# Kernel tuning notes

Measured on AMD Instinct MI355X. Metric: run time of the kernel, lower is better.

The kernel has to match this reference:

```python
import jax, jax.numpy as jnp
import numpy as np

D_MODEL = 2048
D_LATENT = 512
NUM_HEADS = 16
B, T = 2, 2048


def setup_inputs() -> dict:
    key = jax.random.key(0)
    ks = jax.random.split(key, 6)
    s = 0.02  # init scale
    return {
        "x": jax.random.normal(ks[0], (B, T, D_MODEL), jnp.float32),
        # weights stored as [in, out] so y = x @ W (== torch x @ weight.T)
        "w_dkv": jax.random.normal(ks[1], (D_MODEL, D_LATENT), jnp.float32) * s,
        # w_uk kept in torch weight layout [d_model, d_latent] for absorption
        "w_uk": jax.random.normal(ks[2], (D_MODEL, D_LATENT), jnp.float32) * s,
        "w_uv": jax.random.normal(ks[3], (D_LATENT, D_MODEL), jnp.float32) * s,
        "w_q": jax.random.normal(ks[4], (D_MODEL, D_MODEL), jnp.float32) * s,
        "w_o": jax.random.normal(ks[5], (D_MODEL, D_MODEL), jnp.float32) * s,
    }


def reference(x, w_dkv, w_uk, w_uv, w_q, w_o):
    # Eval-mode MLA with weight absorption (w_q_w_uk), dropout is a no-op.
    Bsz, Tl, C = x.shape
    H = NUM_HEADS
    S = C // H
    L = w_dkv.shape[1]
    scale = 1.0 / jnp.sqrt(jnp.asarray(C, x.dtype))

    kv_latent = x @ w_dkv  # [B,T,L]

    # absorbed projection: w_q.T.view(C,H,S) einsum w_uk.view(H,S,L) -> [H,C,L]
    absorbed = jnp.einsum('chs,hsl->hcl', w_q.reshape(C, H, S), w_uk.reshape(H, S, L))

    q_lat = jnp.einsum('btc,hcl->bhtl', x, absorbed)            # [B,H,T,L]
    att = jnp.einsum('bhtl,bsl->bhts', q_lat, kv_latent) * scale  # [B,H,T,T]

    causal_mask = jnp.triu(jnp.ones((Tl, Tl), bool), k=1)
    att = jnp.where(causal_mask, jnp.asarray(-jnp.inf, att.dtype), att)
    att = jax.nn.softmax(att, axis=-1)

    v = (kv_latent @ w_uv).reshape(Bsz, Tl, H, S)               # [B,T,H,S]
    y = jnp.einsum('bhts,bshd->bthd', att, v).reshape(Bsz, Tl, C)
    return y @ w_o
```

## Files before the change

### kernel.cpp

```cpp
#include <hip/hip_runtime.h>
#include <hip/hip_bf16.h>

#define T_SEQ 2048
#define C_DIM 2048
#define L_DIM 512
#define H_NUM 16
#define S_DIM 128
#define B_SZ  2

typedef __attribute__((ext_vector_type(8))) short bf16x8;
typedef __attribute__((ext_vector_type(4))) float f32x4;
typedef __attribute__((ext_vector_type(4))) short short4v;

__device__ inline short f2bf(float f) {
    union { float f; unsigned u; } x; x.f = f;
    unsigned r = x.u + 0x7fffu + ((x.u >> 16) & 1u);
    return (short)(r >> 16);
}

__device__ __forceinline__ void wtile_body(const float* __restrict__ in, short* __restrict__ out,
                                           int R, int C, int r0, int c0, int tid) {
    __shared__ float lds[64][66];
    #pragma unroll
    for (int it = 0; it < 4; it++) {
        int r = (tid >> 4) + it * 16;
        int c4 = (tid & 15) * 4;
        float4 v = *(const float4*)&in[(long)(r0 + r) * C + c0 + c4];
        lds[c4 + 0][r] = v.x; lds[c4 + 1][r] = v.y;
        lds[c4 + 2][r] = v.z; lds[c4 + 3][r] = v.w;
    }
    __syncthreads();
    #pragma unroll
    for (int it = 0; it < 4; it++) {
        int c = tid >> 2;
        int rb = (tid & 3) * 16 + it * 4;
        short4v o;
        #pragma unroll
        for (int j = 0; j < 4; j++) o[j] = f2bf(lds[c][rb + j]);
        *(short4v*)&out[(long)(c0 + c) * R + r0 + rb] = o;
    }
}

__global__ __launch_bounds__(256) void prep_kernel(
    const float* __restrict__ x, short* __restrict__ xb,
    const float* __restrict__ wq, short* __restrict__ wqT,
    const float* __restrict__ wdkv, short* __restrict__ wdkvT,
    const float* __restrict__ wuk, short* __restrict__ wukT,
    const float* __restrict__ wuv, short* __restrict__ wuvT,
    const float* __restrict__ wo, short* __restrict__ woT)
{
    int bid = blockIdx.x, tid = threadIdx.x;
    if (bid < 8192) {
        int i = bid * 256 + tid;
        float4 v = ((const float4*)x)[i];
        short4v o;
        o[0] = f2bf(v.x); o[1] = f2bf(v.y); o[2] = f2bf(v.z); o[3] = f2bf(v.w);
        ((short4v*)xb)[i] = o;
        return;
    }
    int t = bid - 8192;
    if (t < 1024)       wtile_body(wq,   wqT,   2048, 2048, (t >> 5) * 64,            (t & 31) * 64, tid);
    else if (t < 1280)  wtile_body(wdkv, wdkvT, 2048, 512,  ((t - 1024) >> 3) * 64,   ((t - 1024) & 7) * 64, tid);
    else if (t < 1536)  wtile_body(wuk,  wukT,  2048, 512,  ((t - 1280) >> 3) * 64,   ((t - 1280) & 7) * 64, tid);
    else if (t < 1792)  wtile_body(wuv,  wuvT,  512,  2048, ((t - 1536) >> 5) * 64,   ((t - 1536) & 31) * 64, tid);
    else                wtile_body(wo,   woT,   2048, 2048, ((t - 1792) >> 5) * 64,   ((t - 1792) & 31) * 64, tid);
}

__global__ __launch_bounds__(256) void vtrans_kernel(const short* __restrict__ v,
                                                     short* __restrict__ vt) {
    __shared__ short lds[64][68];
    int id = blockIdx.x;
    int b = id >> 10, t2 = id & 1023;
    int t0 = (t2 >> 5) * 64, c0 = (t2 & 31) * 64;
    const short* in = v + (long)b * T_SEQ * C_DIM;
    short* out = vt + (long)b * T_SEQ * C_DIM;
    int tid = threadIdx.x;
    #pragma unroll
    for (int it = 0; it < 4; it++) {
        int t = (tid >> 4) + it * 16;
        int c4 = (tid & 15) * 4;
        short4v vv = *(const short4v*)&in[(long)(t0 + t) * C_DIM + c0 + c4];
        lds[c4 + 0][t] = vv[0]; lds[c4 + 1][t] = vv[1];
        lds[c4 + 2][t] = vv[2]; lds[c4 + 3][t] = vv[3];
    }
    __syncthreads();
    #pragma unroll
    for (int it = 0; it < 4; it++) {
        int c = tid >> 2;
        int tb = (tid & 3) * 16 + it * 4;
        short4v o = *(const short4v*)&lds[c][tb];
        *(short4v*)&out[(long)(c0 + c) * C_DIM + t0 + tb] = o;
    }
}

__device__ __forceinline__ void gemm_body(
    const short* __restrict__ A, const short* __restrict__ Bt,
    float* __restrict__ Cf, short* __restrict__ Cb,
    int K, int lda, int ldb, int ldc, int m0, int n0, long coff, bool outf32, float cscale,
    short (&As)[2][128 * 32], short (&Bs)[2][128 * 32])
{
    int tid = threadIdx.x;
    int wave = tid >> 6, l = tid & 63;
    int wm = (wave >> 1) * 64, wn = (wave & 1) * 64;
    int lr = l & 15, lhi = l >> 4;
    f32x4 acc[4][4] = {};

#define STAGE_AB(KI, BUF) do { \
        _Pragma("unroll") \
        for (int r = 0; r < 2; r++) { \
            int e = (r * 256 + tid) * 8; \
            int row = e >> 5, col = e & 31; \
            __builtin_amdgcn_global_load_lds( \
                (const __attribute__((address_space(1))) unsigned int*)(A + (long)(m0 + row) * lda + (KI) * 32 + col), \
                (__attribute__((address_space(3))) unsigned int*)(&As[BUF][e]), 16, 0, 0); \
            __builtin_amdgcn_global_load_lds( \
                (const __attribute__((address_space(1))) unsigned int*)(Bt + (long)(n0 + row) * ldb + (KI) * 32 + col), \
                (__attribute__((address_space(3))) unsigned int*)(&Bs[BUF][e]), 16, 0, 0); \
        } \
    } while (0)

    int nk = K >> 5;
    STAGE_AB(0, 0);

    for (int i = 0; i < nk; i++) {
        int cur = i & 1;
        asm volatile("s_waitcnt lgkmcnt(0)" ::: "memory");
        __builtin_amdgcn_s_barrier();
        if (i + 1 < nk) {
            STAGE_AB(i + 1, cur ^ 1);
            asm volatile("s_waitcnt vmcnt(4)" ::: "memory");
        } else {
            asm volatile("s_waitcnt vmcnt(0)" ::: "memory");
        }
        __builtin_amdgcn_s_barrier();

        bf16x8 af[4], bfr[4];
        #pragma unroll
        for (int mt = 0; mt < 4; mt++)
            af[mt] = *(const bf16x8*)&As[cur][(wm + mt * 16 + lr) * 32 + lhi * 8];
        #pragma unroll
        for (int nt = 0; nt < 4; nt++)
            bfr[nt] = *(const bf16x8*)&Bs[cur][(wn + nt * 16 + lr) * 32 + lhi * 8];
        #pragma unroll
        for (int mt = 0; mt < 4; mt++)
            #pragma unroll
            for (int nt = 0; nt < 4; nt++)
                acc[mt][nt] = __builtin_amdgcn_mfma_f32_16x16x32_bf16(af[mt], bfr[nt], acc[mt][nt], 0, 0, 0);
    }
#undef STAGE_AB

    #pragma unroll
    for (int mt = 0; mt < 4; mt++) {
        #pragma unroll
        for (int i = 0; i < 4; i++) {
            int row = m0 + wm + mt * 16 + lhi * 4 + i;
            long base = coff + (long)row * ldc + n0 + wn;
            #pragma unroll
            for (int nt = 0; nt < 4; nt++) {
                float val = acc[mt][nt][i] * cscale;
                int colo = nt * 16 + lr;
                if (outf32) Cf[base + colo] = val;
                else        Cb[base + colo] = f2bf(val);
            }
        }
    }
}

__global__ __launch_bounds__(256) void gemm_bt_kernel(
    const short* __restrict__ A, const short* __restrict__ Bt, float* __restrict__ Cf,
    int K, int lda, int ldb, int ldc)
{
    __shared__ __align__(16) short As[2][128 * 32];
    __shared__ __align__(16) short Bs[2][128 * 32];
    int m0 = blockIdx.y * 128, n0 = blockIdx.x * 128;
    gemm_body(A, Bt, Cf, nullptr, K, lda, ldb, ldc, m0, n0, 0, true, 1.0f, As, Bs);
}

__global__ __launch_bounds__(256) void gemm2_kernel(
    const short* A0, const short* Bt0, short* Cb0, int K0, int lda0, int ldb0, int ldc0,
    long sAz0, long sBz0, long sCz0, int nx0, int nxy0, int nblk0, float cscale0,
    const short* A1, const short* Bt1, short* Cb1, int K1, int lda1, int ldb1, int ldc1,
    long sAz1, long sBz1, long sCz1, int nx1, int nxy1, float cscale1)
{
    __shared__ __align__(16) short As[2][128 * 32];
    __shared__ __align__(16) short Bs[2][128 * 32];
    int id = blockIdx.x;
    const short *A, *Bt; short* Cb; int K, lda, ldb, ldc, nx, nxy, local;
    long sAz, sBz, sCz; float cs;
    if (id < nblk0) {
        A = A0; Bt = Bt0; Cb = Cb0; K = K0; lda = lda0; ldb = ldb0; ldc = ldc0;
        sAz = sAz0; sBz = sBz0; sCz = sCz0; nx = nx0; nxy = nxy0; local = id; cs = cscale0;
    } else {
        A = A1; Bt = Bt1; Cb = Cb1; K = K1; lda = lda1; ldb = ldb1; ldc = ldc1;
        sAz = sAz1; sBz = sBz1; sCz = sCz1; nx = nx1; nxy = nxy1; local = id - nblk0; cs = cscale1;
    }
    int z = local / nxy, rem = local % nxy;
    int n0 = (rem % nx) * 128, m0 = (rem / nx) * 128;
    A += (long)z * sAz; Bt += (long)z * sBz;
    gemm_body(A, Bt, nullptr, Cb, K, lda, ldb, ldc, m0, n0, (long)z * sCz, false, cs, As, Bs);
}

__global__ __launch_bounds__(256) void flash13_kernel(
    const short* __restrict__ qlat,
    const short* __restrict__ kv,
    const short* __restrict__ vt,
    short* __restrict__ y)
{
    __shared__ __align__(16) short Ks[32 * 512];
    __shared__ __align__(16) short Ps[4 * 16 * 32];

    int f = blockIdx.x;
    int xcd = f & 7, slot = f >> 3;
    int b = xcd >> 2;
    int h = (xcd & 3) | ((slot >> 4) << 2);
    int pr = slot & 15;
    int tid = threadIdx.x;
    int w = tid >> 6, l = tid & 63, lr = l & 15, lhi = l >> 4;
    const short* qb  = qlat + ((long)(h * B_SZ + b)) * T_SEQ * L_DIM;
    const short* kvb = kv + (long)b * T_SEQ * L_DIM;
    const short* vtb = vt + ((long)(b * H_NUM + h)) * S_DIM * T_SEQ;
    char* Pwb = (char*)(Ps + w * 512);

#define STAGE_K(S0ROW) do { \
        _Pragma("unroll") \
        for (int r = 0; r < 8; r++) { \
            int flat = r * 4096 + tid * 16; \
            int row = flat >> 10, colb = flat & 1023; \
            int src = (((S0ROW) + row) << 10) + (colb ^ ((row & 15) << 4)); \
            __builtin_amdgcn_global_load_lds( \
                (const __attribute__((address_space(1))) unsigned int*)((const char*)kvb + src), \
                (__attribute__((address_space(3))) unsigned int*)((char*)Ks + flat), 16, 0, 0); \
        } \
    } while (0)

    #pragma unroll 1
    for (int sel = 0; sel < 2; sel++) {
        int qt = sel ? pr : (31 - pr);
        int t0 = qt * 64;
        int wt0 = t0 + w * 16;
        int myq = wt0 + lr;

        bf16x8 qf[16];
        #pragma unroll
        for (int ks = 0; ks < 16; ks++)
            qf[ks] = *(const bf16x8*)&qb[(long)(wt0 + lr) * L_DIM + ks * 32 + lhi * 8];

        f32x4 yacc[8] = {};
        float mrun = -__builtin_inff(), lrun = 0.f;

        int nchunk = (t0 >> 5) + 2;

        if (sel == 0) STAGE_K(0);

        for (int c = 0; c < nchunk; c++) {
            int s0 = c * 32;
            asm volatile("s_waitcnt vmcnt(0)" ::: "memory");
            __builtin_amdgcn_s_barrier();

            bool active = (s0 < wt0 + 16);
            bf16x8 vf[8];
            f32x4 sc[2];
            if (active) {
                #pragma unroll
                for (int st = 0; st < 8; st++)
                    vf[st] = *(const bf16x8*)&vtb[(long)(st * 16 + lr) * T_SEQ + s0 + lhi * 8];

                #pragma unroll
                for (int ct = 0; ct < 2; ct++) {
                    int swz = lr << 4;
                    const char* kbase = (const char*)Ks + ((ct * 16 + lr) << 10);
                    f32x4 sA = {}, sB = {};
                    #pragma unroll
                    for (int ks = 0; ks < 8; ks++) {
                        bf16x8 kfA = *(const bf16x8*)(kbase + ((ks * 64 + lhi * 16) ^ swz));
                        bf16x8 kfB = *(const bf16x8*)(kbase + (((ks + 8) * 64 + lhi * 16) ^ swz));
                        sA = __builtin_amdgcn_mfma_f32_16x16x32_bf16(kfA, qf[ks], sA, 0, 0, 0);
                        sB = __builtin_amdgcn_mfma_f32_16x16x32_bf16(kfB, qf[ks + 8], sB, 0, 0, 0);
                    }
                    sc[ct] = sA + sB;
                }
            }
            asm volatile("s_waitcnt lgkmcnt(0)" ::: "memory");
            __builtin_amdgcn_s_barrier();
            if (c + 1 < nchunk) STAGE_K(s0 + 32);

            if (active) {
                float p[2][4];
                #pragma unroll
                for (int sub = 0; sub < 2; sub++)
                    #pragma unroll
                    for (int i = 0; i < 4; i++)
                        p[sub][i] = sc[sub][i];
                if (s0 + 31 > wt0) {
                    #pragma unroll
                    for (int sub = 0; sub < 2; sub++)
                        #pragma unroll
                        for (int i = 0; i < 4; i++) {
                            int kpos = s0 + sub * 16 + lhi * 4 + i;
                            if (kpos > myq) p[sub][i] = -__builtin_inff();
                        }
                }
                float mx = -__builtin_inff();
                #pragma unroll
                for (int sub = 0; sub < 2; sub++)
                    #pragma unroll
                    for (int i = 0; i < 4; i++)
                        mx = fmaxf(mx, p[sub][i]);
                mx = fmaxf(mx, __shfl_xor(mx, 16));
                mx = fmaxf(mx, __shfl_xor(mx, 32));

                unsigned long long grew = __ballot(mx > mrun);
                if (grew) {
                    float mnew = fmaxf(mrun, mx);
                    float fac = exp2f(mrun - mnew);
                    mrun = mnew;
                    lrun *= fac;
                    float facr[4];
                    #pragma unroll
                    for (int i = 0; i < 4; i++)
                        facr[i] = __shfl(fac, lhi * 4 + i);
                    #pragma unroll
                    for (int st = 0; st < 8; st++)
                        #pragma unroll
                        for (int i = 0; i < 4; i++)
                            yacc[st][i] *= facr[i];
                }
                float ls = 0.f;
                #pragma unroll
                for (int sub = 0; sub < 2; sub++)
                    #pragma unroll
                    for (int i = 0; i < 4; i++) {
                        p[sub][i] = exp2f(p[sub][i] - mrun);
                        ls += p[sub][i];
                    }
                ls += __shfl_xor(ls, 16);
                ls += __shfl_xor(ls, 32);
                lrun += ls;

                int swz = (lr & 3) << 4;
                char* pb = Pwb + lr * 64;
                #pragma unroll
                for (int sub = 0; sub < 2; sub++) {
                    short4v pk;
                    #pragma unroll
                    for (int i = 0; i < 4; i++) pk[i] = f2bf(p[sub][i]);
                    *(short4v*)(pb + ((sub * 32 + lhi * 8) ^ swz)) = pk;
                }
                asm volatile("s_waitcnt lgkmcnt(0)" ::: "memory");
                __builtin_amdgcn_sched_barrier(0);
                bf16x8 pf = *(const bf16x8*)(Pwb + lr * 64 + ((lhi * 16) ^ swz));
                #pragma unroll
                for (int st = 0; st < 8; st++)
                    yacc[st] = __builtin_amdgcn_mfma_f32_16x16x32_bf16(pf, vf[st], yacc[st], 0, 0, 0);
            }
        }

        if (sel == 0) STAGE_K(0);

        float lrunr[4];
        #pragma unroll
        for (int i = 0; i < 4; i++)
            lrunr[i] = __shfl(lrun, lhi * 4 + i);
        #pragma unroll
        for (int st = 0; st < 8; st++)
            #pragma unroll
            for (int i = 0; i < 4; i++) {
                int trow = wt0 + lhi * 4 + i;
                float val = yacc[st][i] / lrunr[i];
                y[((long)(b * T_SEQ + trow)) * C_DIM + h * S_DIM + st * 16 + lr] = f2bf(val);
            }
    }
#undef STAGE_K
}

extern "C" void kernel_launch(void* const* d_in, const int* in_sizes, int n_in,
                              void* d_out, int out_size, void* d_ws, size_t ws_size,
                              hipStream_t stream) {
    const float* x    = (const float*)d_in[0];
    const float* wdkv = (const float*)d_in[1];
    const float* wuk  = (const float*)d_in[2];
    const float* wuv  = (const float*)d_in[3];
    const float* wq   = (const float*)d_in[4];
    const float* wo   = (const float*)d_in[5];
    float* out = (float*)d_out;

    short* ws = (short*)d_ws;
    size_t off = 0;
    short* xb    = ws + off; off += (size_t)4096 * 2048;
    short* wqT   = ws + off; off += (size_t)2048 * 2048;
    short* wdkvT = ws + off; off += (size_t)512 * 2048;
    short* wukT  = ws + off; off += (size_t)512 * 2048;
    short* wuvT  = ws + off; off += (size_t)2048 * 512;
    short* woT   = ws + off; off += (size_t)2048 * 2048;
    short* q     = ws + off; off += (size_t)4096 * 2048;
    short* kvb   = ws + off; off += (size_t)4096 * 512;
    short* vbuf  = ws + off; off += (size_t)4096 * 2048;
    short* qlat  = ws + off; off += (size_t)H_NUM * B_SZ * T_SEQ * L_DIM;
    short* vtb  = xb;
    short* ybuf = q;

    const float qscale = 0.022097086912079608f * 1.4426950408889634f;

    prep_kernel<<<11008, 256, 0, stream>>>(x, xb, wq, wqT, wdkv, wdkvT,
                                           wuk, wukT, wuv, wuvT, wo, woT);

    gemm2_kernel<<<640, 256, 0, stream>>>(
        xb, wqT, q, 2048, 2048, 2048, 2048, 0, 0, 0, 16, 512, 512, 1.0f,
        xb, wdkvT, kvb, 2048, 2048, 2048, 512, 0, 0, 0, 4, 128, 1.0f);

    gemm2_kernel<<<2560, 256, 0, stream>>>(
        kvb, wuvT, vbuf, 512, 512, 512, 2048, 0, 0, 0, 16, 512, 512, 1.0f,
        q, wukT, qlat, 128, 2048, 2048, 512, 128, 128, (long)B_SZ * T_SEQ * L_DIM, 4, 128, qscale);

    vtrans_kernel<<<2048, 256, 0, stream>>>(vbuf, vtb);
    flash13_kernel<<<dim3(512, 1, 1), 256, 0, stream>>>(qlat, kvb, vtb, ybuf);
    gemm_bt_kernel<<<dim3(16, 32, 1), 256, 0, stream>>>(ybuf, woT, out, 2048, 2048, 2048, 2048);
}
```

Measured before the change: 357.6 us.

## Fuse V transpose into up-projection GEMM epilogue and raise MFMA priority

The V up-projection GEMM now writes its output transposed through a swizzled LDS staging buffer, so the separate vtrans kernel and its extra 16 MB round trip through global memory are gone. The flash attention kernel also wraps its MFMA blocks in s_setprio to favour matrix issue over other waves. The transposed epilogue adds two block syncs and LDS traffic to that GEMM, and the priority hints may or may not change scheduling.

```diff
diff --git a/kernel.cpp b/kernel.cpp
--- a/kernel.cpp
+++ b/kernel.cpp
@@ -66,38 +66,11 @@
     else                wtile_body(wo,   woT,   2048, 2048, ((t - 1792) >> 5) * 64,   ((t - 1792) & 31) * 64, tid);
 }
 
-__global__ __launch_bounds__(256) void vtrans_kernel(const short* __restrict__ v,
-                                                     short* __restrict__ vt) {
-    __shared__ short lds[64][68];
-    int id = blockIdx.x;
-    int b = id >> 10, t2 = id & 1023;
-    int t0 = (t2 >> 5) * 64, c0 = (t2 & 31) * 64;
-    const short* in = v + (long)b * T_SEQ * C_DIM;
-    short* out = vt + (long)b * T_SEQ * C_DIM;
-    int tid = threadIdx.x;
-    #pragma unroll
-    for (int it = 0; it < 4; it++) {
-        int t = (tid >> 4) + it * 16;
-        int c4 = (tid & 15) * 4;
-        short4v vv = *(const short4v*)&in[(long)(t0 + t) * C_DIM + c0 + c4];
-        lds[c4 + 0][t] = vv[0]; lds[c4 + 1][t] = vv[1];
-        lds[c4 + 2][t] = vv[2]; lds[c4 + 3][t] = vv[3];
-    }
-    __syncthreads();
-    #pragma unroll
-    for (int it = 0; it < 4; it++) {
-        int c = tid >> 2;
-        int tb = (tid & 3) * 16 + it * 4;
-        short4v o = *(const short4v*)&lds[c][tb];
-        *(short4v*)&out[(long)(c0 + c) * C_DIM + t0 + tb] = o;
-    }
-}
-
 __device__ __forceinline__ void gemm_body(
     const short* __restrict__ A, const short* __restrict__ Bt,
     float* __restrict__ Cf, short* __restrict__ Cb,
-    int K, int lda, int ldb, int ldc, int m0, int n0, long coff, bool outf32, float cscale,
-    short (&As)[2][128 * 32], short (&Bs)[2][128 * 32])
+    int K, int lda, int ldb, int ldc, int m0, int n0, long coff, bool outf32, bool transout,
+    float cscale, short (&As)[2][128 * 32], short (&Bs)[2][128 * 32])
 {
     int tid = threadIdx.x;
     int wave = tid >> 6, l = tid & 63;
@@ -149,19 +122,45 @@
     }
 #undef STAGE_AB
 
-    #pragma unroll
-    for (int mt = 0; mt < 4; mt++) {
-        #pragma unroll
-        for (int i = 0; i < 4; i++) {
-            int row = m0 + wm + mt * 16 + lhi * 4 + i;
-            long base = coff + (long)row * ldc + n0 + wn;
+    if (!transout) {
+        #pragma unroll
+        for (int mt = 0; mt < 4; mt++) {
+            #pragma unroll
+            for (int i = 0; i < 4; i++) {
+                int row = m0 + wm + mt * 16 + lhi * 4 + i;
+                long base = coff + (long)row * ldc + n0 + wn;
+                #pragma unroll
+                for (int nt = 0; nt < 4; nt++) {
+                    float val = acc[mt][nt][i] * cscale;
+                    int colo = nt * 16 + lr;
+                    if (outf32) Cf[base + colo] = val;
+                    else        Cb[base + colo] = f2bf(val);
+                }
+            }
+        }
+    } else {
+        __syncthreads();
+        short* sc = &As[0][0];
+        #pragma unroll
+        for (int mt = 0; mt < 4; mt++) {
+            int rowb = wm + mt * 16 + lhi * 4;
             #pragma unroll
             for (int nt = 0; nt < 4; nt++) {
-                float val = acc[mt][nt][i] * cscale;
-                int colo = nt * 16 + lr;
-                if (outf32) Cf[base + colo] = val;
-                else        Cb[base + colo] = f2bf(val);
+                int col = wn + nt * 16 + lr;
+                short4v pk;
+                #pragma unroll
+                for (int i = 0; i < 4; i++) pk[i] = f2bf(acc[mt][nt][i] * cscale);
+                *(short4v*)&sc[col * 128 + (rowb ^ ((col & 7) << 3))] = pk;
             }
+        }
+        __syncthreads();
+        long base = (long)(m0 >> 11) * T_SEQ * C_DIM + (m0 & 2047);
+        #pragma unroll
+        for (int it = 0; it < 8; it++) {
+            int flat = it * 2048 + tid * 8;
+            int col = flat >> 7, rowb = flat & 127;
+            bf16x8 o = *(const bf16x8*)&sc[col * 128 + (rowb ^ ((col & 7) << 3))];
+            *(bf16x8*)&Cb[base + (long)(n0 + col) * T_SEQ + rowb] = o;
         }
     }
 }
@@ -173,31 +172,34 @@
     __shared__ __align__(16) short As[2][128 * 32];
     __shared__ __align__(16) short Bs[2][128 * 32];
     int m0 = blockIdx.y * 128, n0 = blockIdx.x * 128;
-    gemm_body(A, Bt, Cf, nullptr, K, lda, ldb, ldc, m0, n0, 0, true, 1.0f, As, Bs);
+    gemm_body(A, Bt, Cf, nullptr, K, lda, ldb, ldc, m0, n0, 0, true, false, 1.0f, As, Bs);
 }
 
 __global__ __launch_bounds__(256) void gemm2_kernel(
     const short* A0, const short* Bt0, short* Cb0, int K0, int lda0, int ldb0, int ldc0,
-    long sAz0, long sBz0, long sCz0, int nx0, int nxy0, int nblk0, float cscale0,
+    long sAz0, long sBz0, long sCz0, int nx0, int nxy0, int nblk0, float cscale0, int trans0,
     const short* A1, const short* Bt1, short* Cb1, int K1, int lda1, int ldb1, int ldc1,
-    long sAz1, long sBz1, long sCz1, int nx1, int nxy1, float cscale1)
+    long sAz1, long sBz1, long sCz1, int nx1, int nxy1, float cscale1, int trans1)
 {
     __shared__ __align__(16) short As[2][128 * 32];
     __shared__ __align__(16) short Bs[2][128 * 32];
     int id = blockIdx.x;
-    const short *A, *Bt; short* Cb; int K, lda, ldb, ldc, nx, nxy, local;
+    const short *A, *Bt; short* Cb; int K, lda, ldb, ldc, nx, nxy, local, trans;
     long sAz, sBz, sCz; float cs;
     if (id < nblk0) {
         A = A0; Bt = Bt0; Cb = Cb0; K = K0; lda = lda0; ldb = ldb0; ldc = ldc0;
         sAz = sAz0; sBz = sBz0; sCz = sCz0; nx = nx0; nxy = nxy0; local = id; cs = cscale0;
+        trans = trans0;
     } else {
         A = A1; Bt = Bt1; Cb = Cb1; K = K1; lda = lda1; ldb = ldb1; ldc = ldc1;
         sAz = sAz1; sBz = sBz1; sCz = sCz1; nx = nx1; nxy = nxy1; local = id - nblk0; cs = cscale1;
+        trans = trans1;
     }
     int z = local / nxy, rem = local % nxy;
     int n0 = (rem % nx) * 128, m0 = (rem / nx) * 128;
     A += (long)z * sAz; Bt += (long)z * sBz;
-    gemm_body(A, Bt, nullptr, Cb, K, lda, ldb, ldc, m0, n0, (long)z * sCz, false, cs, As, Bs);
+    gemm_body(A, Bt, nullptr, Cb, K, lda, ldb, ldc, m0, n0, (long)z * sCz, false, trans != 0,
+              cs, As, Bs);
 }
 
 __global__ __launch_bounds__(256) void flash13_kernel(
@@ -265,6 +267,7 @@
                 for (int st = 0; st < 8; st++)
                     vf[st] = *(const bf16x8*)&vtb[(long)(st * 16 + lr) * T_SEQ + s0 + lhi * 8];
 
+                __builtin_amdgcn_s_setprio(1);
                 #pragma unroll
                 for (int ct = 0; ct < 2; ct++) {
                     int swz = lr << 4;
@@ -279,6 +282,7 @@
                     }
                     sc[ct] = sA + sB;
                 }
+                __builtin_amdgcn_s_setprio(0);
             }
             asm volatile("s_waitcnt lgkmcnt(0)" ::: "memory");
             __builtin_amdgcn_s_barrier();
@@ -349,9 +353,11 @@
                 asm volatile("s_waitcnt lgkmcnt(0)" ::: "memory");
                 __builtin_amdgcn_sched_barrier(0);
                 bf16x8 pf = *(const bf16x8*)(Pwb + lr * 64 + ((lhi * 16) ^ swz));
+                __builtin_amdgcn_s_setprio(1);
                 #pragma unroll
                 for (int st = 0; st < 8; st++)
                     yacc[st] = __builtin_amdgcn_mfma_f32_16x16x32_bf16(pf, vf[st], yacc[st], 0, 0, 0);
+                __builtin_amdgcn_s_setprio(0);
             }
         }
 
@@ -398,6 +404,7 @@
     short* qlat  = ws + off; off += (size_t)H_NUM * B_SZ * T_SEQ * L_DIM;
     short* vtb  = xb;
     short* ybuf = q;
+    (void)vbuf;
 
     const float qscale = 0.022097086912079608f * 1.4426950408889634f;
 
@@ -405,14 +412,13 @@
                                            wuk, wukT, wuv, wuvT, wo, woT);
 
     gemm2_kernel<<<640, 256, 0, stream>>>(
-        xb, wqT, q, 2048, 2048, 2048, 2048, 0, 0, 0, 16, 512, 512, 1.0f,
-        xb, wdkvT, kvb, 2048, 2048, 2048, 512, 0, 0, 0, 4, 128, 1.0f);
+        xb, wqT, q, 2048, 2048, 2048, 2048, 0, 0, 0, 16, 512, 512, 1.0f, 0,
+        xb, wdkvT, kvb, 2048, 2048, 2048, 512, 0, 0, 0, 4, 128, 1.0f, 0);
 
     gemm2_kernel<<<2560, 256, 0, stream>>>(
-        kvb, wuvT, vbuf, 512, 512, 512, 2048, 0, 0, 0, 16, 512, 512, 1.0f,
-        q, wukT, qlat, 128, 2048, 2048, 512, 128, 128, (long)B_SZ * T_SEQ * L_DIM, 4, 128, qscale);
-
-    vtrans_kernel<<<2048, 256, 0, stream>>>(vbuf, vtb);
+        kvb, wuvT, vtb, 512, 512, 512, 2048, 0, 0, 0, 16, 512, 512, 1.0f, 1,
+        q, wukT, qlat, 128, 2048, 2048, 512, 128, 128, (long)B_SZ * T_SEQ * L_DIM, 4, 128, qscale, 0);
+
     flash13_kernel<<<dim3(512, 1, 1), 256, 0, stream>>>(qlat, kvb, vtb, ybuf);
     gemm_bt_kernel<<<dim3(16, 32, 1), 256, 0, stream>>>(ybuf, woT, out, 2048, 2048, 2048, 2048);
 }
```

Result: slower. 371.9 us (+4.0%).
